# Kernel optimization log

Hardware: AMD Instinct MI355X
Metric: run time of the kernel (lower is better)

Reference implementation:

```python
import jax, jax.numpy as jnp
import numpy as np

B, S, D, H = 2, 2048, 2048, 16
HD = D // H  # head_dim = 128


def setup_inputs() -> dict:
    key = jax.random.key(0)
    ks = jax.random.split(key, 10)
    sc = 1.0 / np.sqrt(D)
    inp = {
        "hidden_states": jax.random.normal(ks[0], (B, S, D), dtype=jnp.float32),
        "attention_mask": jnp.zeros((B, 1, S, S), dtype=jnp.float32),
        "Wq": jax.random.normal(ks[1], (D, D), dtype=jnp.float32) * sc,
        "bq": jnp.zeros((D,), dtype=jnp.float32),
        "Wk": jax.random.normal(ks[2], (D, D), dtype=jnp.float32) * sc,
        "bk": jnp.zeros((D,), dtype=jnp.float32),
        "Wv": jax.random.normal(ks[3], (D, D), dtype=jnp.float32) * sc,
        "bv": jnp.zeros((D,), dtype=jnp.float32),
        "Wo": jax.random.normal(ks[4], (D, D), dtype=jnp.float32) * sc,
        "bo": jnp.zeros((D,), dtype=jnp.float32),
    }
    return inp


def reference(hidden_states, attention_mask, Wq, bq, Wk, bk, Wv, bv, Wo, bo):
    # torch Linear: y = x @ W^T + b
    q = hidden_states @ Wq.T + bq
    k = hidden_states @ Wk.T + bk
    v = hidden_states @ Wv.T + bv
    # [B,S,D] -> [B,H,S,HD]
    q = q.reshape(B, S, H, HD).transpose(0, 2, 1, 3)
    k = k.reshape(B, S, H, HD).transpose(0, 2, 1, 3)
    v = v.reshape(B, S, H, HD).transpose(0, 2, 1, 3)
    # RoPE in source is an identity passthrough; apply_rotary_pos_emb returns (q, k) unchanged.
    scores = jnp.einsum("bhqd,bhkd->bhqk", q, k) / jnp.sqrt(jnp.float32(HD))
    scores = scores + attention_mask  # broadcast over heads
    attn = jax.nn.softmax(scores, axis=-1)
    out = jnp.einsum("bhqk,bhkd->bhqd", attn, v)
    out = out.transpose(0, 2, 1, 3).reshape(B, S, D)
    return out @ Wo.T + bo
```

## Files before the change

### kernel.cpp

```cpp
#include <hip/hip_runtime.h>
#include <hip/hip_bf16.h>
#include <math.h>

typedef unsigned short u16;
typedef unsigned int u32;
typedef __attribute__((ext_vector_type(8))) short bf16x8;
typedef __attribute__((ext_vector_type(4))) float f32x4;

constexpr int Bc = 2, Sc = 2048, Dc = 2048, Hc = 16, HDc = 128;
constexpr int Mc = Bc * Sc;
constexpr float SCALE = 0.08838834764831845f;

__device__ inline u16 f2bf(float f) {
  __hip_bfloat16 h = __float2bfloat16(f);
  return __builtin_bit_cast(u16, h);
}

typedef const __attribute__((address_space(1))) u32 glb_u32;
typedef __attribute__((address_space(3))) u32 lds_u32;
__device__ inline void gload16(const void* g, void* l) {
  __builtin_amdgcn_global_load_lds((glb_u32*)g, (lds_u32*)l, 16, 0, 0);
}

__global__ __launch_bounds__(256) void cvt5(
    const float* __restrict__ s0, u16* __restrict__ d0, int n0,
    const float* __restrict__ s1, u16* __restrict__ d1, int n1,
    const float* __restrict__ s2, u16* __restrict__ d2, int n2,
    const float* __restrict__ s3, u16* __restrict__ d3, int n3,
    const float* __restrict__ s4, u16* __restrict__ d4, int n4) {
  int i = blockIdx.x * 256 + threadIdx.x;
  const float* s; u16* d;
  if (i < n0) { s = s0; d = d0; }
  else { i -= n0;
    if (i < n1) { s = s1; d = d1; }
    else { i -= n1;
      if (i < n2) { s = s2; d = d2; }
      else { i -= n2;
        if (i < n3) { s = s3; d = d3; }
        else { i -= n3;
          if (i >= n4) return;
          s = s4; d = d4; } } } }
  float4 v = reinterpret_cast<const float4*>(s)[i];
  ushort4 o;
  o.x = f2bf(v.x); o.y = f2bf(v.y); o.z = f2bf(v.z); o.w = f2bf(v.w);
  reinterpret_cast<ushort4*>(d)[i] = o;
}

constexpr int GBM = 128, GBN = 128, GBK = 64;

template <int MODE>
__global__ __launch_bounds__(256) void gemm_bf16(
    const u16* __restrict__ A, const u16* __restrict__ W,
    const float* __restrict__ bias, void* __restrict__ outp, float scale) {
  __shared__ u16 smem[17408];
  u16* As = smem;
  u16* Bs = smem + 8192;
  char* Asb = (char*)As;
  char* Bsb = (char*)Bs;
  const int t = threadIdx.x;
  const int w = t >> 6, lane = t & 63, g = lane >> 4, c = lane & 15;
  const int wm = w >> 1, wn = w & 1;
  const int m0 = blockIdx.y * GBM, n0 = blockIdx.x * GBN;

  f32x4 acc[4][4];
#pragma unroll
  for (int m = 0; m < 4; ++m)
#pragma unroll
    for (int n = 0; n < 4; ++n) acc[m][n] = 0.f;

  for (int k0 = 0; k0 < Dc; k0 += GBK) {
#pragma unroll
    for (int i = 0; i < 4; ++i) {
      int u = i * 256 + t;
      int row = u >> 3, cu = u & 7;
      int ub = i * 256 + (t & 192);
      gload16(A + (size_t)(m0 + row) * Dc + k0 + cu * 8, Asb + ub * 16);
      gload16(W + (size_t)(n0 + row) * Dc + k0 + cu * 8, Bsb + ub * 16);
    }
    __syncthreads();
#pragma unroll
    for (int s = 0; s < 2; ++s) {
      bf16x8 af[4], bfv[4];
#pragma unroll
      for (int m = 0; m < 4; ++m)
        af[m] = *(const bf16x8*)(Asb + (wm * 64 + m * 16 + c) * 128 + s * 64 + g * 16);
#pragma unroll
      for (int n = 0; n < 4; ++n)
        bfv[n] = *(const bf16x8*)(Bsb + (wn * 64 + n * 16 + c) * 128 + s * 64 + g * 16);
#pragma unroll
      for (int m = 0; m < 4; ++m)
#pragma unroll
        for (int n = 0; n < 4; ++n)
          acc[m][n] = __builtin_amdgcn_mfma_f32_16x16x32_bf16(af[m], bfv[n], acc[m][n], 0, 0, 0);
    }
    __syncthreads();
  }

  if (MODE == 2) {
    u16* CT = smem;
    __syncthreads();
#pragma unroll
    for (int m = 0; m < 4; ++m)
#pragma unroll
      for (int n = 0; n < 4; ++n) {
        int lcol = wn * 64 + n * 16 + c;
        float bv = bias[n0 + lcol];
#pragma unroll
        for (int r = 0; r < 4; ++r) {
          int lrow = wm * 64 + m * 16 + g * 4 + r;
          CT[lcol * 136 + lrow] = f2bf(acc[m][n][r] + bv);
        }
      }
    __syncthreads();
    const int b = m0 >> 11, h = n0 >> 7, s0 = m0 & (Sc - 1);
    u16* op = (u16*)outp;
#pragma unroll
    for (int i = 0; i < 8; ++i) {
      int u = i * 256 + t;
      int d = u >> 4, su = u & 15;
      size_t gbase = ((size_t)((b * Hc + h) * HDc) + d) * Sc + s0;
#pragma unroll
      for (int p2 = 0; p2 < 4; ++p2) {
        int sl = su * 8 + p2 * 2;
        u32 val = (u32)CT[d * 136 + sl] | ((u32)CT[d * 136 + sl + 1] << 16);
        int w6 = sl & 63, blk = sl >> 6;
        int slot = ((w6 >> 5) << 5) | (((w6 >> 2) & 3) << 3) |
                   (((w6 >> 4) & 1) << 2) | (w6 & 3);
        *(u32*)&op[gbase + blk * 64 + slot] = val;
      }
    }
    return;
  }

#pragma unroll
  for (int m = 0; m < 4; ++m)
#pragma unroll
    for (int n = 0; n < 4; ++n) {
      int col = n0 + wn * 64 + n * 16 + c;
      float bv = bias[col];
#pragma unroll
      for (int r = 0; r < 4; ++r) {
        int row = m0 + wm * 64 + m * 16 + g * 4 + r;
        float v = (acc[m][n][r] + bv) * scale;
        if (MODE == 0) {
          int b = row >> 11, si = row & (Sc - 1);
          int h = col >> 7, d = col & (HDc - 1);
          ((u16*)outp)[((size_t)((b * Hc + h) * Sc + si)) * HDc + d] = f2bf(v);
        } else {
          ((float*)outp)[(size_t)row * Dc + col] = v;
        }
      }
    }
}

__global__ __launch_bounds__(128, 2) void attn_mfma(
    const u16* __restrict__ Q, const u16* __restrict__ K,
    const u16* __restrict__ VT, const float* __restrict__ mask,
    u16* __restrict__ outb) {
  __shared__ u16 Ks[64 * 128];
  __shared__ u16 Vt[128 * 64];
  char* Ksb = (char*)Ks;
  char* Vtb = (char*)Vt;
  const int t = threadIdx.x, w = t >> 6, lane = t & 63, g = lane >> 4, c = lane & 15;
  const int bid = blockIdx.x;
  const int nid = (bid & 7) * 128 + (bid >> 3);
  const int bh = nid >> 5;
  const int q0 = (nid & 31) * 64;
  const int bq = bh >> 4, h = bh & 15;
  const u16* Qp = Q + ((size_t)bh << 18);
  const u16* Kp = K + ((size_t)bh << 18);
  const u16* VTp = VT + ((size_t)bh << 18);

  bf16x8 qf0[4], qf1[4];
  {
    int qr0 = q0 + w * 32 + c;
    int qr1 = qr0 + 16;
#pragma unroll
    for (int d0 = 0; d0 < 4; ++d0) {
      qf0[d0] = *(const bf16x8*)(Qp + (size_t)qr0 * HDc + d0 * 32 + g * 8);
      qf1[d0] = *(const bf16x8*)(Qp + (size_t)qr1 * HDc + d0 * 32 + g * 8);
    }
  }

  f32x4 po0[8], po1[8];
#pragma unroll
  for (int m = 0; m < 8; ++m) { po0[m] = 0.f; po1[m] = 0.f; }
  float lsum0 = 0.f, lsum1 = 0.f;
  const float* mrow0 = mask + ((size_t)bq * Sc + q0 + w * 32 + c) * Sc;
  const float* mrow1 = mrow0 + (size_t)16 * Sc;

#pragma unroll 1
  for (int kt = 0; kt < 32; ++kt) {
    const int k0 = kt * 64;
#pragma unroll
    for (int i = 0; i < 8; ++i) {
      int u = i * 128 + t, row = u >> 4, p = u & 15;
      int cu = (p & 8) | ((p ^ row) & 7);
      gload16(Kp + (size_t)(k0 + row) * HDc + cu * 8,
              Ksb + (i * 128 + (t & 64)) * 16);
    }
#pragma unroll
    for (int i = 0; i < 8; ++i) {
      int u = i * 128 + t, d = u >> 3, p = u & 7;
      int cu = (p ^ d) & 7;
      gload16(VTp + (size_t)d * Sc + k0 + cu * 8,
              Vtb + (i * 128 + (t & 64)) * 16);
    }
    float4 mk0[4], mk1[4];
#pragma unroll
    for (int n = 0; n < 4; ++n) {
      mk0[n] = *(const float4*)(mrow0 + k0 + n * 16 + g * 4);
      mk1[n] = *(const float4*)(mrow1 + k0 + n * 16 + g * 4);
    }
    __syncthreads();

    f32x4 sfr0[4], sfr1[4];
#pragma unroll
    for (int n = 0; n < 4; ++n) { sfr0[n] = 0.f; sfr1[n] = 0.f; }
    __builtin_amdgcn_s_setprio(1);
#pragma unroll
    for (int ds = 0; ds < 4; ++ds)
#pragma unroll
      for (int n = 0; n < 4; ++n) {
        int row = n * 16 + c;
        int cu = ds * 4 + g;
        int scu = (cu & 8) | ((cu ^ row) & 7);
        bf16x8 kf = *(const bf16x8*)(Ksb + row * 256 + scu * 16);
        sfr0[n] = __builtin_amdgcn_mfma_f32_16x16x32_bf16(kf, qf0[ds], sfr0[n], 0, 0, 0);
        sfr1[n] = __builtin_amdgcn_mfma_f32_16x16x32_bf16(kf, qf1[ds], sfr1[n], 0, 0, 0);
      }
    __builtin_amdgcn_s_setprio(0);

    u32 a01[4], a23[4], b01[4], b23[4];
#pragma unroll
    for (int n = 0; n < 4; ++n) {
      float p0 = __expf(sfr0[n][0] + mk0[n].x);
      float p1 = __expf(sfr0[n][1] + mk0[n].y);
      float p2 = __expf(sfr0[n][2] + mk0[n].z);
      float p3 = __expf(sfr0[n][3] + mk0[n].w);
      lsum0 += (p0 + p1) + (p2 + p3);
      a01[n] = (u32)f2bf(p0) | ((u32)f2bf(p1) << 16);
      a23[n] = (u32)f2bf(p2) | ((u32)f2bf(p3) << 16);
      float r0 = __expf(sfr1[n][0] + mk1[n].x);
      float r1 = __expf(sfr1[n][1] + mk1[n].y);
      float r2 = __expf(sfr1[n][2] + mk1[n].z);
      float r3 = __expf(sfr1[n][3] + mk1[n].w);
      lsum1 += (r0 + r1) + (r2 + r3);
      b01[n] = (u32)f2bf(r0) | ((u32)f2bf(r1) << 16);
      b23[n] = (u32)f2bf(r2) | ((u32)f2bf(r3) << 16);
    }

    __builtin_amdgcn_s_setprio(1);
#pragma unroll
    for (int s2 = 0; s2 < 2; ++s2) {
      uint4 pw0, pw1;
      pw0.x = a01[s2 * 2]; pw0.y = a23[s2 * 2];
      pw0.z = a01[s2 * 2 + 1]; pw0.w = a23[s2 * 2 + 1];
      pw1.x = b01[s2 * 2]; pw1.y = b23[s2 * 2];
      pw1.z = b01[s2 * 2 + 1]; pw1.w = b23[s2 * 2 + 1];
      bf16x8 pf0 = __builtin_bit_cast(bf16x8, pw0);
      bf16x8 pf1 = __builtin_bit_cast(bf16x8, pw1);
#pragma unroll
      for (int m = 0; m < 8; ++m) {
        int d = m * 16 + c;
        int scuv = ((s2 * 4 + g) ^ (d & 7)) & 7;
        bf16x8 vf = *(const bf16x8*)(Vtb + d * 128 + scuv * 16);
        po0[m] = __builtin_amdgcn_mfma_f32_16x16x32_bf16(vf, pf0, po0[m], 0, 0, 0);
        po1[m] = __builtin_amdgcn_mfma_f32_16x16x32_bf16(vf, pf1, po1[m], 0, 0, 0);
      }
    }
    __builtin_amdgcn_s_setprio(0);
    __syncthreads();
  }

  lsum0 += __shfl_xor(lsum0, 16, 64);
  lsum0 += __shfl_xor(lsum0, 32, 64);
  lsum1 += __shfl_xor(lsum1, 16, 64);
  lsum1 += __shfl_xor(lsum1, 32, 64);
  const float rl0 = 1.0f / lsum0;
  const float rl1 = 1.0f / lsum1;
  const int qg0 = q0 + w * 32 + c;
  u16* ob0 = outb + ((size_t)(bq * Sc + qg0)) * Dc + h * HDc;
  u16* ob1 = ob0 + (size_t)16 * Dc;
#pragma unroll
  for (int m = 0; m < 8; ++m) {
    ushort4 o4;
    o4.x = f2bf(po0[m][0] * rl0);
    o4.y = f2bf(po0[m][1] * rl0);
    o4.z = f2bf(po0[m][2] * rl0);
    o4.w = f2bf(po0[m][3] * rl0);
    *(ushort4*)(ob0 + m * 16 + g * 4) = o4;
    ushort4 o5;
    o5.x = f2bf(po1[m][0] * rl1);
    o5.y = f2bf(po1[m][1] * rl1);
    o5.z = f2bf(po1[m][2] * rl1);
    o5.w = f2bf(po1[m][3] * rl1);
    *(ushort4*)(ob1 + m * 16 + g * 4) = o5;
  }
}

extern "C" void kernel_launch(void* const* d_in, const int* in_sizes, int n_in,
                              void* d_out, int out_size, void* d_ws,
                              size_t ws_size, hipStream_t stream) {
  const float* hs   = (const float*)d_in[0];
  const float* mask = (const float*)d_in[1];
  const float* Wq   = (const float*)d_in[2];
  const float* bqp  = (const float*)d_in[3];
  const float* Wk   = (const float*)d_in[4];
  const float* bkp  = (const float*)d_in[5];
  const float* Wv   = (const float*)d_in[6];
  const float* bvp  = (const float*)d_in[7];
  const float* Wo   = (const float*)d_in[8];
  const float* bop  = (const float*)d_in[9];

  u16* Xb  = (u16*)d_ws;
  u16* Wqb = Xb + (size_t)Mc * Dc;
  u16* Wkb = Wqb + (size_t)Dc * Dc;
  u16* Wvb = Wkb + (size_t)Dc * Dc;
  u16* Wob = Wvb + (size_t)Dc * Dc;
  u16* qb  = Wob + (size_t)Dc * Dc;
  u16* kb  = qb + (size_t)Mc * Dc;
  u16* vtb = kb + (size_t)Mc * Dc;
  u16* ab  = vtb + (size_t)Mc * Dc;

  const int nh4 = Mc * Dc / 4;
  const int nw4 = Dc * Dc / 4;
  cvt5<<<dim3((nh4 + 4 * nw4) / 256), dim3(256), 0, stream>>>(
      hs, Xb, nh4, Wq, Wqb, nw4, Wk, Wkb, nw4, Wv, Wvb, nw4, Wo, Wob, nw4);

  dim3 blk(256);
  dim3 gg(Dc / GBN, Mc / GBM);
  gemm_bf16<0><<<gg, blk, 0, stream>>>(Xb, Wqb, bqp, qb, SCALE);
  gemm_bf16<0><<<gg, blk, 0, stream>>>(Xb, Wkb, bkp, kb, 1.0f);
  gemm_bf16<2><<<gg, blk, 0, stream>>>(Xb, Wvb, bvp, vtb, 1.0f);
  attn_mfma<<<dim3(1024), dim3(128), 0, stream>>>(qb, kb, vtb, mask, ab);
  gemm_bf16<1><<<gg, blk, 0, stream>>>(ab, Wob, bop, d_out, 1.0f);
}
```

Before: 324.0 us.

## Double-buffer K/V tiles in attention and use exp2 with log2e-folded Q scale

```diff
diff --git a/kernel.cpp b/kernel.cpp
--- a/kernel.cpp
+++ b/kernel.cpp
@@ -10,6 +10,7 @@
 constexpr int Bc = 2, Sc = 2048, Dc = 2048, Hc = 16, HDc = 128;
 constexpr int Mc = Bc * Sc;
 constexpr float SCALE = 0.08838834764831845f;
+constexpr float LOG2E = 1.4426950408889634f;
 
 __device__ inline u16 f2bf(float f) {
   __hip_bfloat16 h = __float2bfloat16(f);
@@ -153,14 +154,12 @@
     }
 }
 
-__global__ __launch_bounds__(128, 2) void attn_mfma(
+__global__ __launch_bounds__(128) void attn_mfma(
     const u16* __restrict__ Q, const u16* __restrict__ K,
     const u16* __restrict__ VT, const float* __restrict__ mask,
     u16* __restrict__ outb) {
-  __shared__ u16 Ks[64 * 128];
-  __shared__ u16 Vt[128 * 64];
-  char* Ksb = (char*)Ks;
-  char* Vtb = (char*)Vt;
+  __shared__ u16 Ks[2][64 * 128];
+  __shared__ u16 Vt[2][64 * 128];
   const int t = threadIdx.x, w = t >> 6, lane = t & 63, g = lane >> 4, c = lane & 15;
   const int bid = blockIdx.x;
   const int nid = (bid & 7) * 128 + (bid >> 3);
@@ -171,14 +170,25 @@
   const u16* Kp = K + ((size_t)bh << 18);
   const u16* VTp = VT + ((size_t)bh << 18);
 
+  const u16* kSrc[8];
+  const u16* vSrc[8];
+#pragma unroll
+  for (int i = 0; i < 8; ++i) {
+    int u = i * 128 + t, row = u >> 4, p = u & 15;
+    int cu = (p & 8) | ((p ^ row) & 7);
+    kSrc[i] = Kp + (size_t)row * HDc + cu * 8;
+    int d = u >> 3, pv = u & 7;
+    int cv = (pv ^ d) & 7;
+    vSrc[i] = VTp + (size_t)d * Sc + cv * 8;
+  }
+
   bf16x8 qf0[4], qf1[4];
   {
     int qr0 = q0 + w * 32 + c;
-    int qr1 = qr0 + 16;
 #pragma unroll
     for (int d0 = 0; d0 < 4; ++d0) {
       qf0[d0] = *(const bf16x8*)(Qp + (size_t)qr0 * HDc + d0 * 32 + g * 8);
-      qf1[d0] = *(const bf16x8*)(Qp + (size_t)qr1 * HDc + d0 * 32 + g * 8);
+      qf1[d0] = *(const bf16x8*)(Qp + (size_t)(qr0 + 16) * HDc + d0 * 32 + g * 8);
     }
   }
 
@@ -189,30 +199,34 @@
   const float* mrow0 = mask + ((size_t)bq * Sc + q0 + w * 32 + c) * Sc;
   const float* mrow1 = mrow0 + (size_t)16 * Sc;
 
+  auto STAGE = [&](int buf) {
+#pragma unroll
+    for (int i = 0; i < 8; ++i)
+      gload16(kSrc[i], (char*)Ks + buf * 16384 + (i * 128 + (t & 64)) * 16);
+#pragma unroll
+    for (int i = 0; i < 8; ++i)
+      gload16(vSrc[i], (char*)Vt + buf * 16384 + (i * 128 + (t & 64)) * 16);
+#pragma unroll
+    for (int i = 0; i < 8; ++i) { kSrc[i] += 64 * HDc; vSrc[i] += 64; }
+  };
+
+  STAGE(0);
+  __syncthreads();
+  int buf = 0;
+
 #pragma unroll 1
   for (int kt = 0; kt < 32; ++kt) {
     const int k0 = kt * 64;
-#pragma unroll
-    for (int i = 0; i < 8; ++i) {
-      int u = i * 128 + t, row = u >> 4, p = u & 15;
-      int cu = (p & 8) | ((p ^ row) & 7);
-      gload16(Kp + (size_t)(k0 + row) * HDc + cu * 8,
-              Ksb + (i * 128 + (t & 64)) * 16);
-    }
-#pragma unroll
-    for (int i = 0; i < 8; ++i) {
-      int u = i * 128 + t, d = u >> 3, p = u & 7;
-      int cu = (p ^ d) & 7;
-      gload16(VTp + (size_t)d * Sc + k0 + cu * 8,
-              Vtb + (i * 128 + (t & 64)) * 16);
-    }
     float4 mk0[4], mk1[4];
 #pragma unroll
     for (int n = 0; n < 4; ++n) {
       mk0[n] = *(const float4*)(mrow0 + k0 + n * 16 + g * 4);
       mk1[n] = *(const float4*)(mrow1 + k0 + n * 16 + g * 4);
     }
-    __syncthreads();
+    if (kt + 1 < 32) STAGE(buf ^ 1);
+
+    const char* Ksb = (const char*)Ks + buf * 16384;
+    const char* Vtb = (const char*)Vt + buf * 16384;
 
     f32x4 sfr0[4], sfr1[4];
 #pragma unroll
@@ -234,17 +248,17 @@
     u32 a01[4], a23[4], b01[4], b23[4];
 #pragma unroll
     for (int n = 0; n < 4; ++n) {
-      float p0 = __expf(sfr0[n][0] + mk0[n].x);
-      float p1 = __expf(sfr0[n][1] + mk0[n].y);
-      float p2 = __expf(sfr0[n][2] + mk0[n].z);
-      float p3 = __expf(sfr0[n][3] + mk0[n].w);
+      float p0 = __builtin_amdgcn_exp2f(fmaf(mk0[n].x, LOG2E, sfr0[n][0]));
+      float p1 = __builtin_amdgcn_exp2f(fmaf(mk0[n].y, LOG2E, sfr0[n][1]));
+      float p2 = __builtin_amdgcn_exp2f(fmaf(mk0[n].z, LOG2E, sfr0[n][2]));
+      float p3 = __builtin_amdgcn_exp2f(fmaf(mk0[n].w, LOG2E, sfr0[n][3]));
       lsum0 += (p0 + p1) + (p2 + p3);
       a01[n] = (u32)f2bf(p0) | ((u32)f2bf(p1) << 16);
       a23[n] = (u32)f2bf(p2) | ((u32)f2bf(p3) << 16);
-      float r0 = __expf(sfr1[n][0] + mk1[n].x);
-      float r1 = __expf(sfr1[n][1] + mk1[n].y);
-      float r2 = __expf(sfr1[n][2] + mk1[n].z);
-      float r3 = __expf(sfr1[n][3] + mk1[n].w);
+      float r0 = __builtin_amdgcn_exp2f(fmaf(mk1[n].x, LOG2E, sfr1[n][0]));
+      float r1 = __builtin_amdgcn_exp2f(fmaf(mk1[n].y, LOG2E, sfr1[n][1]));
+      float r2 = __builtin_amdgcn_exp2f(fmaf(mk1[n].z, LOG2E, sfr1[n][2]));
+      float r3 = __builtin_amdgcn_exp2f(fmaf(mk1[n].w, LOG2E, sfr1[n][3]));
       lsum1 += (r0 + r1) + (r2 + r3);
       b01[n] = (u32)f2bf(r0) | ((u32)f2bf(r1) << 16);
       b23[n] = (u32)f2bf(r2) | ((u32)f2bf(r3) << 16);
@@ -271,6 +285,7 @@
     }
     __builtin_amdgcn_s_setprio(0);
     __syncthreads();
+    buf ^= 1;
   }
 
   lsum0 += __shfl_xor(lsum0, 16, 64);
@@ -330,7 +345,7 @@
 
   dim3 blk(256);
   dim3 gg(Dc / GBN, Mc / GBM);
-  gemm_bf16<0><<<gg, blk, 0, stream>>>(Xb, Wqb, bqp, qb, SCALE);
+  gemm_bf16<0><<<gg, blk, 0, stream>>>(Xb, Wqb, bqp, qb, SCALE * LOG2E);
   gemm_bf16<0><<<gg, blk, 0, stream>>>(Xb, Wkb, bkp, kb, 1.0f);
   gemm_bf16<2><<<gg, blk, 0, stream>>>(Xb, Wvb, bvp, vtb, 1.0f);
   attn_mfma<<<dim3(1024), dim3(128), 0, stream>>>(qb, kb, vtb, mask, ab);
```

Measured after the change: 360.1 us. 1.11x slower.
